# Performance work log

Measured on AMD Instinct MI355X. Metric: run time of the kernel, lower is better.

The kernel has to match this reference:

```python
import jax, jax.numpy as jnp
import numpy as np

LRELU_SLOPE = 0.2
FUSED_SCALE = float(np.sqrt(2.0))


def _haar_kernels():
    l = np.ones((1, 2), np.float32) / np.sqrt(np.float32(2.0))
    h = l.copy()
    h[0, 0] = -h[0, 0]
    ll = l.T @ l
    lh = h.T @ l
    hl = l.T @ h
    hh = h.T @ h
    return jnp.asarray(ll), jnp.asarray(lh), jnp.asarray(hl), jnp.asarray(hh)


def _blur_kernel():
    k = np.array([1.0, 3.0, 3.0, 1.0], np.float32)
    k = np.outer(k, k)
    k = k / k.sum()
    return jnp.asarray(k)


def upfirdn2d(x, k, up=1, down=1, pad=(0, 0)):
    """Faithful upfirdn2d: zero-upsample by `up`, pad, FIR filter (true
    convolution, i.e. flipped kernel), then stride-`down` decimation.
    Implemented as a single lax conv with lhs_dilation; the extra (up-1)
    trailing pad reproduces torch's H*up zero-padded upsampling."""
    if len(pad) == 2:
        px0, px1, py0, py1 = pad[0], pad[1], pad[0], pad[1]
    else:
        px0, px1, py0, py1 = pad
    B, C, H, W = x.shape
    w = jnp.flip(k, (0, 1))[None, None].astype(x.dtype)  # [1,1,kh,kw]
    out = jax.lax.conv_general_dilated(
        x.reshape(B * C, 1, H, W), w,
        window_strides=(down, down),
        padding=((py0, py1 + up - 1), (px0, px1 + up - 1)),
        lhs_dilation=(up, up),
        dimension_numbers=('NCHW', 'OIHW', 'NCHW'))
    return out.reshape(B, C, out.shape[2], out.shape[3])


def setup_inputs() -> dict:
    key = jax.random.key(0)
    k1, k2 = jax.random.split(key)
    B, C_wt, H, W = 32, 12, 256, 256
    out_channel = 256
    x = jax.random.normal(k1, (B, C_wt, H, W), dtype=jnp.float32)
    weight = jax.random.normal(k2, (out_channel, C_wt, 1, 1), dtype=jnp.float32)
    bias = jnp.zeros((out_channel,), dtype=jnp.float32)
    return {"x": x, "weight": weight, "bias": bias}


def reference(x, weight, bias):
    ll, lh, hl, hh = _haar_kernels()
    c = x.shape[1] // 4
    # InverseHaarTransform (iwt kernels: ll, -lh, -hl, hh), up=2, pad=(1,0,1,0)
    parts = (x[:, 0*c:1*c], x[:, 1*c:2*c], x[:, 2*c:3*c], x[:, 3*c:4*c])
    kerns = (ll, -lh, -hl, hh)
    y = upfirdn2d(parts[0], kerns[0], up=2, pad=(1, 0, 1, 0))
    for p, kk in zip(parts[1:], kerns[1:]):
        y = y + upfirdn2d(p, kk, up=2, pad=(1, 0, 1, 0))
    # Downsample: blur kernel [1,3,3,1], factor=2 -> pad=(1,1), down=2
    y = upfirdn2d(y, _blur_kernel(), down=2, pad=(1, 1))
    # HaarTransform: down=2, pad=(0,0)
    t = jnp.concatenate([upfirdn2d(y, kk, down=2) for kk in (ll, lh, hl, hh)], axis=1)
    # EqualConv2d 1x1 (scale = 1/sqrt(in_channel*k^2), no conv bias) + FusedLeakyReLU
    scale = 1.0 / np.sqrt(np.float32(weight.shape[1]))  # kernel_size = 1
    out = jnp.einsum('bchw,oc->bohw', t, weight[:, :, 0, 0] * scale)
    out = jax.nn.leaky_relu(out + bias[None, :, None, None], LRELU_SLOPE) * FUSED_SCALE
    return t, out
```

## Files before the change

### kernel.cpp

```cpp
#include <hip/hip_runtime.h>


#define T_ELEMS 6291456
#define HW_T    16384
#define HW_X    65536

typedef float f4v __attribute__((ext_vector_type(4)));

__global__ __launch_bounds__(256) void fused_fromrgb_kernel(
    const float* __restrict__ x, const float* __restrict__ w,
    const float* __restrict__ bias, float* __restrict__ t,
    float* __restrict__ out)
{
    __shared__ float ws[256 * 12];
    __shared__ float bs[256];
    const int tid = threadIdx.x;

    const float wscale = 0.2886751345948129f;
    bs[tid] = bias[tid];
    #pragma unroll
    for (int i = 0; i < 12; ++i)
        ws[i * 256 + tid] = w[i * 256 + tid] * wscale;

    const int q   = tid & 31;
    const int ur  = tid >> 5;
    const int u   = blockIdx.x * 8 + ur;
    const int b   = blockIdx.y;

    const float F[2][2][4] = {
        { { 1.f,  7.f,  7.f,  1.f}, {-1.f, -1.f, 1.f,  1.f} },
        { { 1.f,  5.f, -5.f, -1.f}, {-1.f,  1.f, 1.f, -1.f} }
    };

    const int r0    = 2 * u - 1;
    const int cbase = 8 * q;

    float tv[12][4];

    #pragma unroll
    for (int ch = 0; ch < 3; ++ch) {
        float acc[4][4];
        #pragma unroll
        for (int k = 0; k < 4; ++k)
            #pragma unroll
            for (int p = 0; p < 4; ++p) acc[k][p] = 0.f;

        #pragma unroll
        for (int g = 0; g < 4; ++g) {
            const int gr = g & 1, gc = g >> 1;
            const float* xp = x + ((size_t)(b * 12 + g * 3 + ch)) * HW_X;
            #pragma unroll
            for (int dy = 0; dy < 4; ++dy) {
                const int r = r0 + dy;
                float c[10];
                if (r >= 0 && r < 256) {
                    const float* rp = xp + (r << 8) + cbase;
                    const float4 A = *reinterpret_cast<const float4*>(rp);
                    const float4 B = *reinterpret_cast<const float4*>(rp + 4);
                    c[1] = A.x; c[2] = A.y; c[3] = A.z; c[4] = A.w;
                    c[5] = B.x; c[6] = B.y; c[7] = B.z; c[8] = B.w;
                    float left = 0.f, right = 0.f;
                    if (q > 0)  left  = rp[-1];
                    if (q < 31) right = rp[8];
                    c[0] = left; c[9] = right;
                } else {
                    #pragma unroll
                    for (int i = 0; i < 10; ++i) c[i] = 0.f;
                }
                #pragma unroll
                for (int p = 0; p < 4; ++p) {
                    float s0 = 0.f, s1 = 0.f;
                    #pragma unroll
                    for (int dx = 0; dx < 4; ++dx) {
                        s0 = fmaf(F[0][gc][dx], c[2 * p + dx], s0);
                        s1 = fmaf(F[1][gc][dx], c[2 * p + dx], s1);
                    }
                    acc[0][p] = fmaf(F[0][gr][dy], s0, acc[0][p]);
                    acc[1][p] = fmaf(F[1][gr][dy], s0, acc[1][p]);
                    acc[2][p] = fmaf(F[0][gr][dy], s1, acc[2][p]);
                    acc[3][p] = fmaf(F[1][gr][dy], s1, acc[3][p]);
                }
            }
        }

        const float sc = 1.f / 256.f;
        #pragma unroll
        for (int k = 0; k < 4; ++k) {
            f4v o;
            o.x = acc[k][0] * sc; o.y = acc[k][1] * sc;
            o.z = acc[k][2] * sc; o.w = acc[k][3] * sc;
            tv[k * 3 + ch][0] = o.x; tv[k * 3 + ch][1] = o.y;
            tv[k * 3 + ch][2] = o.z; tv[k * 3 + ch][3] = o.w;
            __builtin_nontemporal_store(o, reinterpret_cast<f4v*>(
                t + ((size_t)(b * 12 + k * 3 + ch)) * HW_T + (u << 7) + 4 * q));
        }
    }

    __syncthreads();

    const float SQ2 = 1.4142135623730951f;
    const int base = (u << 7) + 4 * q;
    float* outp = out + ((size_t)b * 256) * HW_T + base;

    #pragma unroll 2
    for (int oo = 0; oo < 256; ++oo) {
        const float4 w0 = *reinterpret_cast<const float4*>(&ws[oo * 12 + 0]);
        const float4 w1 = *reinterpret_cast<const float4*>(&ws[oo * 12 + 4]);
        const float4 w2 = *reinterpret_cast<const float4*>(&ws[oo * 12 + 8]);
        const float bo = bs[oo];
        float a0 = bo, a1 = bo, a2 = bo, a3 = bo;
        #pragma unroll
        for (int c = 0; c < 4; ++c) {
            const float wv = (&w0.x)[c];
            a0 = fmaf(tv[c][0], wv, a0); a1 = fmaf(tv[c][1], wv, a1);
            a2 = fmaf(tv[c][2], wv, a2); a3 = fmaf(tv[c][3], wv, a3);
        }
        #pragma unroll
        for (int c = 0; c < 4; ++c) {
            const float wv = (&w1.x)[c];
            a0 = fmaf(tv[c + 4][0], wv, a0); a1 = fmaf(tv[c + 4][1], wv, a1);
            a2 = fmaf(tv[c + 4][2], wv, a2); a3 = fmaf(tv[c + 4][3], wv, a3);
        }
        #pragma unroll
        for (int c = 0; c < 4; ++c) {
            const float wv = (&w2.x)[c];
            a0 = fmaf(tv[c + 8][0], wv, a0); a1 = fmaf(tv[c + 8][1], wv, a1);
            a2 = fmaf(tv[c + 8][2], wv, a2); a3 = fmaf(tv[c + 8][3], wv, a3);
        }
        f4v av;
        av.x = fmaxf(a0, 0.2f * a0) * SQ2;
        av.y = fmaxf(a1, 0.2f * a1) * SQ2;
        av.z = fmaxf(a2, 0.2f * a2) * SQ2;
        av.w = fmaxf(a3, 0.2f * a3) * SQ2;
        __builtin_nontemporal_store(
            av, reinterpret_cast<f4v*>(outp + (size_t)oo * HW_T));
    }
}

extern "C" void kernel_launch(void* const* d_in, const int* in_sizes, int n_in,
                              void* d_out, int out_size, void* d_ws, size_t ws_size,
                              hipStream_t stream) {
    const float* x    = (const float*)d_in[0];
    const float* wgt  = (const float*)d_in[1];
    const float* bias = (const float*)d_in[2];
    float* t   = (float*)d_out;
    float* out = t + T_ELEMS;

    dim3 blk(256, 1, 1), grd(16, 32, 1);
    hipLaunchKernelGGL(fused_fromrgb_kernel, grd, blk, 0, stream,
                       x, wgt, bias, t, out);
}
```

Baseline: 132.7 us.

## Halve per-thread output width and double grid to raise parallelism

Each thread now computes 2 output columns instead of 4, with 64 threads per output row and 4 rows per block, and the grid doubles to 1024 blocks. The goal is more resident waves and lower per-thread register use (tv shrinks to 12x2) so the memory-bound 1x1-conv store loop has more parallelism to hide latency. In exchange, stores narrow from 16-byte to 8-byte vectors, the weight table is loaded into shared memory twice as many times, and halo loads grow relative to useful data.

```diff
diff --git a/kernel.cpp b/kernel.cpp
--- a/kernel.cpp
+++ b/kernel.cpp
@@ -5,7 +5,7 @@
 #define HW_T    16384
 #define HW_X    65536
 
-typedef float f4v __attribute__((ext_vector_type(4)));
+typedef float f2v __attribute__((ext_vector_type(2)));
 
 __global__ __launch_bounds__(256) void fused_fromrgb_kernel(
     const float* __restrict__ x, const float* __restrict__ w,
@@ -22,10 +22,10 @@
     for (int i = 0; i < 12; ++i)
         ws[i * 256 + tid] = w[i * 256 + tid] * wscale;
 
-    const int q   = tid & 31;
-    const int ur  = tid >> 5;
-    const int u   = blockIdx.x * 8 + ur;
-    const int b   = blockIdx.y;
+    const int l  = tid & 63;
+    const int ur = tid >> 6;
+    const int u  = blockIdx.x * 4 + ur;
+    const int b  = blockIdx.y;
 
     const float F[2][2][4] = {
         { { 1.f,  7.f,  7.f,  1.f}, {-1.f, -1.f, 1.f,  1.f} },
@@ -33,17 +33,15 @@
     };
 
     const int r0    = 2 * u - 1;
-    const int cbase = 8 * q;
+    const int cbase = 4 * l;
 
-    float tv[12][4];
+    float tv[12][2];
 
     #pragma unroll
     for (int ch = 0; ch < 3; ++ch) {
-        float acc[4][4];
+        float acc[4][2];
         #pragma unroll
-        for (int k = 0; k < 4; ++k)
-            #pragma unroll
-            for (int p = 0; p < 4; ++p) acc[k][p] = 0.f;
+        for (int k = 0; k < 4; ++k) { acc[k][0] = 0.f; acc[k][1] = 0.f; }
 
         #pragma unroll
         for (int g = 0; g < 4; ++g) {
@@ -52,23 +50,19 @@
             #pragma unroll
             for (int dy = 0; dy < 4; ++dy) {
                 const int r = r0 + dy;
-                float c[10];
+                float c[6];
                 if (r >= 0 && r < 256) {
                     const float* rp = xp + (r << 8) + cbase;
                     const float4 A = *reinterpret_cast<const float4*>(rp);
-                    const float4 B = *reinterpret_cast<const float4*>(rp + 4);
                     c[1] = A.x; c[2] = A.y; c[3] = A.z; c[4] = A.w;
-                    c[5] = B.x; c[6] = B.y; c[7] = B.z; c[8] = B.w;
-                    float left = 0.f, right = 0.f;
-                    if (q > 0)  left  = rp[-1];
-                    if (q < 31) right = rp[8];
-                    c[0] = left; c[9] = right;
+                    c[0] = (l > 0)  ? rp[-1] : 0.f;
+                    c[5] = (l < 63) ? rp[4]  : 0.f;
                 } else {
                     #pragma unroll
-                    for (int i = 0; i < 10; ++i) c[i] = 0.f;
+                    for (int i = 0; i < 6; ++i) c[i] = 0.f;
                 }
                 #pragma unroll
-                for (int p = 0; p < 4; ++p) {
+                for (int p = 0; p < 2; ++p) {
                     float s0 = 0.f, s1 = 0.f;
                     #pragma unroll
                     for (int dx = 0; dx < 4; ++dx) {
@@ -86,54 +80,47 @@
         const float sc = 1.f / 256.f;
         #pragma unroll
         for (int k = 0; k < 4; ++k) {
-            f4v o;
+            f2v o;
             o.x = acc[k][0] * sc; o.y = acc[k][1] * sc;
-            o.z = acc[k][2] * sc; o.w = acc[k][3] * sc;
             tv[k * 3 + ch][0] = o.x; tv[k * 3 + ch][1] = o.y;
-            tv[k * 3 + ch][2] = o.z; tv[k * 3 + ch][3] = o.w;
-            __builtin_nontemporal_store(o, reinterpret_cast<f4v*>(
-                t + ((size_t)(b * 12 + k * 3 + ch)) * HW_T + (u << 7) + 4 * q));
+            __builtin_nontemporal_store(o, reinterpret_cast<f2v*>(
+                t + ((size_t)(b * 12 + k * 3 + ch)) * HW_T + (u << 7) + 2 * l));
         }
     }
 
     __syncthreads();
 
     const float SQ2 = 1.4142135623730951f;
-    const int base = (u << 7) + 4 * q;
+    const int base = (u << 7) + 2 * l;
     float* outp = out + ((size_t)b * 256) * HW_T + base;
 
-    #pragma unroll 2
+    #pragma unroll 4
     for (int oo = 0; oo < 256; ++oo) {
         const float4 w0 = *reinterpret_cast<const float4*>(&ws[oo * 12 + 0]);
         const float4 w1 = *reinterpret_cast<const float4*>(&ws[oo * 12 + 4]);
         const float4 w2 = *reinterpret_cast<const float4*>(&ws[oo * 12 + 8]);
         const float bo = bs[oo];
-        float a0 = bo, a1 = bo, a2 = bo, a3 = bo;
+        float a0 = bo, a1 = bo;
         #pragma unroll
         for (int c = 0; c < 4; ++c) {
             const float wv = (&w0.x)[c];
             a0 = fmaf(tv[c][0], wv, a0); a1 = fmaf(tv[c][1], wv, a1);
-            a2 = fmaf(tv[c][2], wv, a2); a3 = fmaf(tv[c][3], wv, a3);
         }
         #pragma unroll
         for (int c = 0; c < 4; ++c) {
             const float wv = (&w1.x)[c];
             a0 = fmaf(tv[c + 4][0], wv, a0); a1 = fmaf(tv[c + 4][1], wv, a1);
-            a2 = fmaf(tv[c + 4][2], wv, a2); a3 = fmaf(tv[c + 4][3], wv, a3);
         }
         #pragma unroll
         for (int c = 0; c < 4; ++c) {
             const float wv = (&w2.x)[c];
             a0 = fmaf(tv[c + 8][0], wv, a0); a1 = fmaf(tv[c + 8][1], wv, a1);
-            a2 = fmaf(tv[c + 8][2], wv, a2); a3 = fmaf(tv[c + 8][3], wv, a3);
         }
-        f4v av;
+        f2v av;
         av.x = fmaxf(a0, 0.2f * a0) * SQ2;
         av.y = fmaxf(a1, 0.2f * a1) * SQ2;
-        av.z = fmaxf(a2, 0.2f * a2) * SQ2;
-        av.w = fmaxf(a3, 0.2f * a3) * SQ2;
         __builtin_nontemporal_store(
-            av, reinterpret_cast<f4v*>(outp + (size_t)oo * HW_T));
+            av, reinterpret_cast<f2v*>(outp + (size_t)oo * HW_T));
     }
 }
 
@@ -146,7 +133,7 @@
     float* t   = (float*)d_out;
     float* out = t + T_ELEMS;
 
-    dim3 blk(256, 1, 1), grd(16, 32, 1);
+    dim3 blk(256, 1, 1), grd(32, 32, 1);
     hipLaunchKernelGGL(fused_fromrgb_kernel, grd, blk, 0, stream,
                        x, wgt, bias, t, out);
 }
```

After: 129.8 us, median of 2. -2.2%, faster.
